# Kernel optimization log

Hardware: AMD Instinct MI355X
Metric: run time of the kernel (lower is better)

The kernel has to match this reference:

```python
import jax, jax.numpy as jnp
import numpy as np

BATCH = 256
INPUT_DIM = 64
LEVELS = 100
HV_DIM = 10000


def setup_inputs() -> dict:
    key = jax.random.key(0)
    kx, kb = jax.random.split(key)
    x = jax.random.uniform(kx, (BATCH, INPUT_DIM), dtype=jnp.float32)
    base = jax.random.normal(kb, (INPUT_DIM, LEVELS, HV_DIM), dtype=jnp.float32)
    # buffer is L2-normalized along hv_dim at construction time
    base = base / jnp.linalg.norm(base, axis=-1, keepdims=True)
    return {"x": x, "base_hvs": base}


def reference(x, base_hvs):
    D, L, H = base_hvs.shape
    B = x.shape[0]
    xn = jnp.clip(x * (L - 1), 0.0, float(L - 1))          # [B, D]
    lo = jnp.floor(xn).astype(jnp.int32)                    # [B, D]
    hi = jnp.clip(lo + 1, 0, L - 1)                         # [B, D]
    alpha = xn - lo.astype(x.dtype)                         # [B, D]

    def step(acc, inputs):
        bhv, l, h, a = inputs    # bhv: [L, H], l/h/a: [B]
        hv_low = bhv[l]          # [B, H] gather
        hv_high = bhv[h]         # [B, H] gather
        a = a[:, None]
        return acc + (1.0 - a) * hv_low + a * hv_high, None

    init = jnp.zeros((B, H), dtype=x.dtype)
    encoded, _ = jax.lax.scan(step, init, (base_hvs, lo.T, hi.T, alpha.T))
    return encoded / jnp.linalg.norm(encoded, axis=-1, keepdims=True)
```

## Files before the change

### kernel.cpp

```cpp
#include <hip/hip_runtime.h>
#include <hip/hip_fp16.h>
#include <hip/hip_bf16.h>

#define BATCH   256
#define DIMS    64
#define LEVELS  100
#define HVD     10000
#define WH      32
#define NHT     313
#define DSPLIT  4
#define DPER    16
#define NBUF    3
#define TPB     256
#define FTPB    1024
#define CHUNK_FLOATS (LEVELS * WH)
#define NSTG    13

typedef unsigned int   uint;
typedef unsigned short ushort;
typedef unsigned char  uchar;


static __device__ __forceinline__ ushort f2bf(float f) {
    __hip_bfloat16 h = __float2bfloat16(f);
    return *reinterpret_cast<ushort*>(&h);
}

__global__ __launch_bounds__(TPB, 3) void encode_kernel(
    const float* __restrict__ x,
    const float* __restrict__ base,
    ushort*     __restrict__ partial)
{
    __shared__ float  s_buf[NBUF][CHUNK_FLOATS];
    __shared__ ushort s_alpha[DPER][BATCH];
    __shared__ uchar  s_lo[DPER][BATCH];

    const int tid   = threadIdx.x;
    const int w     = tid >> 6;
    const int lane  = tid & 63;
    const int htile = blockIdx.x;
    const int split = blockIdx.y;
    const int h0    = htile * WH;
    const int d0    = split * DPER;
    const int wvalid = (HVD - h0) < WH ? (HVD - h0) : WH;

    {
        const float4* xr = (const float4*)(x + (size_t)tid * DIMS + d0);
        const float4 x0 = xr[0];
        const float4 x1 = xr[1];
        const float4 x2 = xr[2];
        const float4 x3 = xr[3];
        const float xv[16] = { x0.x, x0.y, x0.z, x0.w, x1.x, x1.y, x1.z, x1.w,
                               x2.x, x2.y, x2.z, x2.w, x3.x, x3.y, x3.z, x3.w };
        #pragma unroll
        for (int k = 0; k < DPER; ++k) {
            float xn = fminf(fmaxf(xv[k] * (float)(LEVELS - 1), 0.0f),
                             (float)(LEVELS - 1));
            float fl = floorf(xn);
            int   lo = (int)fl;
            s_alpha[k][tid] = (ushort)__half_as_ushort(__float2half(xn - fl));
            s_lo[k][tid]    = (uchar)lo;
        }
    }
    __syncthreads();

    const int srow = lane >> 3;
    const int scol = (lane & 7) * 4;
    const float* srcdim = base + (size_t)d0 * LEVELS * HVD + h0;

    auto issue_chunk = [&](int dc, int bufidx) {
        const float* src = srcdim + (size_t)dc * LEVELS * HVD;
        float* dst = &s_buf[bufidx][0];
        for (int p = w; p < NSTG; p += 4) {
            const int row = 8 * p + srow;
            const float* g = src + (size_t)row * HVD + scol;
            if (row < LEVELS && scol < wvalid) {
                __builtin_amdgcn_global_load_lds(
                    (const __attribute__((address_space(1))) uint*)g,
                    (__attribute__((address_space(3))) uint*)(dst + p * 8 * WH),
                    16, 0, 0);
            }
        }
    };

    issue_chunk(0, 0);
    issue_chunk(1, 1);
    issue_chunk(2, 2);

    const int sub   = lane >> 4;
    const int p2    = lane & 15;
    const int pb    = p2 * 8;
    const int bbase = w * 64;

    float2 acc[16];
    #pragma unroll
    for (int j = 0; j < 16; ++j) acc[j] = make_float2(0.f, 0.f);

    int cur = 0;
    #pragma unroll 1
    for (int dc = 0; dc < DPER; ++dc) {
        if (dc < DPER - 2)       asm volatile("s_waitcnt vmcnt(6)" ::: "memory");
        else if (dc == DPER - 2) asm volatile("s_waitcnt vmcnt(3)" ::: "memory");
        else                     asm volatile("s_waitcnt vmcnt(0)" ::: "memory");
        __builtin_amdgcn_s_barrier();

        const char* buf = (const char*)&s_buf[cur][0];
        #pragma unroll
        for (int j = 0; j < 16; ++j) {
            const uint2 av = *(const uint2*)&s_alpha[dc][bbase + 4 * j];
            const uint  lv = *(const uint*)&s_lo[dc][bbase + 4 * j];
            const uint  aw = (sub & 2) ? av.y : av.x;
            const float a  = __half2float(__ushort_as_half(
                                (ushort)((sub & 1) ? (aw >> 16) : (aw & 0xffffu))));
            const int olo = (int)((lv >> (8 * sub)) & 0xffu) << 7;
            const int ohi = min(olo + 128, (LEVELS - 1) << 7);
            const float2 vlo = *(const float2*)(buf + olo + pb);
            const float2 vhi = *(const float2*)(buf + ohi + pb);
            const float wl = 1.0f - a;
            acc[j].x += wl * vlo.x + a * vhi.x;
            acc[j].y += wl * vlo.y + a * vhi.y;
        }
        asm volatile("" ::: "memory");
        __builtin_amdgcn_s_barrier();
        if (dc + NBUF < DPER) issue_chunk(dc + NBUF, cur);
        cur = (cur == NBUF - 1) ? 0 : cur + 1;
    }

    if (p2 * 2 < wvalid) {
        #pragma unroll
        for (int j = 0; j < 16; ++j) {
            const int b = bbase + 4 * j + sub;
            const uint pk = (uint)f2bf(acc[j].x) | ((uint)f2bf(acc[j].y) << 16);
            *(uint*)(partial + ((size_t)split * BATCH + b) * (size_t)HVD + h0 + p2 * 2) = pk;
        }
    }
}

__global__ __launch_bounds__(FTPB) void finish_kernel(
    const ushort* __restrict__ partial,
    float* __restrict__ out)
{
    const int b   = blockIdx.x;
    const int tid = threadIdx.x;

    float4 v0[2], v1[2];
    float  ss = 0.f;
    #pragma unroll
    for (int k = 0; k < 2; ++k) {
        const int g = k * FTPB + tid;
        float4 a = make_float4(0.f, 0.f, 0.f, 0.f);
        float4 c = make_float4(0.f, 0.f, 0.f, 0.f);
        if (g < HVD / 8) {
            #pragma unroll
            for (int sp = 0; sp < DSPLIT; ++sp) {
                const uint4 u = *(const uint4*)(partial +
                    ((size_t)sp * BATCH + b) * (size_t)HVD + (size_t)g * 8);
                a.x += __uint_as_float(u.x << 16);
                a.y += __uint_as_float(u.x & 0xffff0000u);
                a.z += __uint_as_float(u.y << 16);
                a.w += __uint_as_float(u.y & 0xffff0000u);
                c.x += __uint_as_float(u.z << 16);
                c.y += __uint_as_float(u.z & 0xffff0000u);
                c.z += __uint_as_float(u.w << 16);
                c.w += __uint_as_float(u.w & 0xffff0000u);
            }
            ss += a.x * a.x + a.y * a.y + a.z * a.z + a.w * a.w
                + c.x * c.x + c.y * c.y + c.z * c.z + c.w * c.w;
        }
        v0[k] = a; v1[k] = c;
    }

    __shared__ float red[FTPB];
    red[tid] = ss;
    __syncthreads();
    #pragma unroll
    for (int sh = FTPB / 2; sh > 0; sh >>= 1) {
        if (tid < sh) red[tid] += red[tid + sh];
        __syncthreads();
    }
    const float inv = rsqrtf(red[0]);

    #pragma unroll
    for (int k = 0; k < 2; ++k) {
        const int g = k * FTPB + tid;
        if (g < HVD / 8) {
            float4 a = v0[k], c = v1[k];
            a.x *= inv; a.y *= inv; a.z *= inv; a.w *= inv;
            c.x *= inv; c.y *= inv; c.z *= inv; c.w *= inv;
            *(float4*)(out + (size_t)b * HVD + (size_t)g * 8)     = a;
            *(float4*)(out + (size_t)b * HVD + (size_t)g * 8 + 4) = c;
        }
    }
}

extern "C" void kernel_launch(void* const* d_in, const int* in_sizes, int n_in,
                              void* d_out, int out_size, void* d_ws, size_t ws_size,
                              hipStream_t stream)
{
    const float* x    = (const float*)d_in[0];
    const float* base = (const float*)d_in[1];
    float*       out  = (float*)d_out;
    ushort*      part = (ushort*)d_ws;

    dim3 grid(NHT, DSPLIT);
    encode_kernel<<<grid, TPB, 0, stream>>>(x, base, part);
    finish_kernel<<<BATCH, FTPB, 0, stream>>>(part, out);
}
```

Measured before the change: 372.3 us.

## Overlap x preprocessing with prefetch, single-barrier pipeline, shuffle-based norm reduction

Issues the x loads and the first two base-chunk async LDS loads before computing the per-batch alpha/lo tables, so global latency overlaps that setup work. The main loop moves from prefetch depth 3 with two barriers per chunk to prefetch depth 2 with one barrier per chunk, issuing the next chunk right after the barrier. The vmcnt thresholds now depend on the wave, since wave 0 issues one extra load per chunk. The finish kernel replaces a 1024-entry shared-memory tree reduction with wave shuffles plus a small cross-wave step. The risks are less prefetch slack and subtle correctness around buffer reuse, because one barrier now has to guard both the reads of the old buffer and the writes into it.

```diff
diff --git a/kernel.cpp b/kernel.cpp
--- a/kernel.cpp
+++ b/kernel.cpp
@@ -44,26 +44,6 @@
     const int d0    = split * DPER;
     const int wvalid = (HVD - h0) < WH ? (HVD - h0) : WH;
 
-    {
-        const float4* xr = (const float4*)(x + (size_t)tid * DIMS + d0);
-        const float4 x0 = xr[0];
-        const float4 x1 = xr[1];
-        const float4 x2 = xr[2];
-        const float4 x3 = xr[3];
-        const float xv[16] = { x0.x, x0.y, x0.z, x0.w, x1.x, x1.y, x1.z, x1.w,
-                               x2.x, x2.y, x2.z, x2.w, x3.x, x3.y, x3.z, x3.w };
-        #pragma unroll
-        for (int k = 0; k < DPER; ++k) {
-            float xn = fminf(fmaxf(xv[k] * (float)(LEVELS - 1), 0.0f),
-                             (float)(LEVELS - 1));
-            float fl = floorf(xn);
-            int   lo = (int)fl;
-            s_alpha[k][tid] = (ushort)__half_as_ushort(__float2half(xn - fl));
-            s_lo[k][tid]    = (uchar)lo;
-        }
-    }
-    __syncthreads();
-
     const int srow = lane >> 3;
     const int scol = (lane & 7) * 4;
     const float* srcdim = base + (size_t)d0 * LEVELS * HVD + h0;
@@ -83,9 +63,31 @@
         }
     };
 
+    const float4* xr = (const float4*)(x + (size_t)tid * DIMS + d0);
+    const float4 x0 = xr[0];
+    const float4 x1 = xr[1];
+    const float4 x2 = xr[2];
+    const float4 x3 = xr[3];
+    __builtin_amdgcn_sched_barrier(0);
+
     issue_chunk(0, 0);
     issue_chunk(1, 1);
-    issue_chunk(2, 2);
+    __builtin_amdgcn_sched_barrier(0);
+
+    {
+        const float xv[16] = { x0.x, x0.y, x0.z, x0.w, x1.x, x1.y, x1.z, x1.w,
+                               x2.x, x2.y, x2.z, x2.w, x3.x, x3.y, x3.z, x3.w };
+        #pragma unroll
+        for (int k = 0; k < DPER; ++k) {
+            float xn = fminf(fmaxf(xv[k] * (float)(LEVELS - 1), 0.0f),
+                             (float)(LEVELS - 1));
+            float fl = floorf(xn);
+            s_alpha[k][tid] = (ushort)__half_as_ushort(__float2half(xn - fl));
+            s_lo[k][tid]    = (uchar)(int)fl;
+        }
+    }
+    asm volatile("s_waitcnt lgkmcnt(0)" ::: "memory");
+    __builtin_amdgcn_sched_barrier(0);
 
     const int sub   = lane >> 4;
     const int p2    = lane & 15;
@@ -99,10 +101,18 @@
     int cur = 0;
     #pragma unroll 1
     for (int dc = 0; dc < DPER; ++dc) {
-        if (dc < DPER - 2)       asm volatile("s_waitcnt vmcnt(6)" ::: "memory");
-        else if (dc == DPER - 2) asm volatile("s_waitcnt vmcnt(3)" ::: "memory");
-        else                     asm volatile("s_waitcnt vmcnt(0)" ::: "memory");
+        if (dc < DPER - 1) {
+            if (w == 0) asm volatile("s_waitcnt vmcnt(4)" ::: "memory");
+            else        asm volatile("s_waitcnt vmcnt(3)" ::: "memory");
+        } else {
+            asm volatile("s_waitcnt vmcnt(0)" ::: "memory");
+        }
         __builtin_amdgcn_s_barrier();
+
+        if (dc + 2 < DPER) {
+            int tgt = cur + 2; if (tgt >= NBUF) tgt -= NBUF;
+            issue_chunk(dc + 2, tgt);
+        }
 
         const char* buf = (const char*)&s_buf[cur][0];
         #pragma unroll
@@ -120,9 +130,7 @@
             acc[j].x += wl * vlo.x + a * vhi.x;
             acc[j].y += wl * vlo.y + a * vhi.y;
         }
-        asm volatile("" ::: "memory");
-        __builtin_amdgcn_s_barrier();
-        if (dc + NBUF < DPER) issue_chunk(dc + NBUF, cur);
+        asm volatile("s_waitcnt lgkmcnt(0)" ::: "memory");
         cur = (cur == NBUF - 1) ? 0 : cur + 1;
     }
 
@@ -140,8 +148,10 @@
     const ushort* __restrict__ partial,
     float* __restrict__ out)
 {
-    const int b   = blockIdx.x;
-    const int tid = threadIdx.x;
+    const int b    = blockIdx.x;
+    const int tid  = threadIdx.x;
+    const int wid  = tid >> 6;
+    const int lane = tid & 63;
 
     float4 v0[2], v1[2];
     float  ss = 0.f;
@@ -170,14 +180,19 @@
         v0[k] = a; v1[k] = c;
     }
 
-    __shared__ float red[FTPB];
-    red[tid] = ss;
+    #pragma unroll
+    for (int off = 32; off > 0; off >>= 1) ss += __shfl_down(ss, off, 64);
+
+    __shared__ float red[FTPB / 64];
+    if (lane == 0) red[wid] = ss;
     __syncthreads();
-    #pragma unroll
-    for (int sh = FTPB / 2; sh > 0; sh >>= 1) {
-        if (tid < sh) red[tid] += red[tid + sh];
-        __syncthreads();
-    }
+    if (wid == 0) {
+        float v = (lane < FTPB / 64) ? red[lane] : 0.f;
+        #pragma unroll
+        for (int off = 8; off > 0; off >>= 1) v += __shfl_down(v, off, 64);
+        if (lane == 0) red[0] = v;
+    }
+    __syncthreads();
     const float inv = rsqrtf(red[0]);
 
     #pragma unroll
```

Result: no change. 371.6 us (-0.2%).
